# Kernel optimization log

Measured on AMD Instinct MI355X. Metric: run time of the kernel, lower is better.

Reference implementation:

```python
import jax, jax.numpy as jnp
import numpy as np

B, T, D, U, R = 64, 512, 256, 256, 4


def setup_inputs() -> dict:
    key = jax.random.key(0)
    ks = jax.random.split(key, 12)
    inputs = jax.random.normal(ks[0], (B, T, D), dtype=jnp.float32)
    # per-timestep dependency indices into past timesteps; must satisfy dep[t] <= t
    dependencies = jnp.minimum(
        jax.random.randint(ks[1], (T, R - 1), 0, T), jnp.arange(T)[:, None]
    ).astype(jnp.int32)
    mask = jax.random.randint(ks[2], (B, T), 0, 2).astype(jnp.int32)
    initial_states = jax.random.normal(ks[3], (R, B, U), dtype=jnp.float32) * 0.1
    s = 1.0 / np.sqrt(U)
    def w(k, shape):
        return jax.random.normal(k, shape, dtype=jnp.float32) * s
    return dict(
        inputs=inputs, dependencies=dependencies, mask=mask, initial_states=initial_states,
        Wz=w(ks[4], (D, U)), Wr=w(ks[5], (D, U)), Wh=w(ks[6], (D, U)),
        Uz=w(ks[7], (U, U)), Ur=w(ks[8], (U, U)), Uh=w(ks[9], (U, U)),
        bz=jnp.zeros((U,), jnp.float32), br=jnp.zeros((U,), jnp.float32), bh=jnp.zeros((U,), jnp.float32),
    )


def reference(inputs, dependencies, mask, initial_states, Wz, Wr, Wh, Uz, Ur, Uh, bz, br, bh):
    Bn, Tn, _ = inputs.shape
    Rn = initial_states.shape[0]
    Un = Uz.shape[0]

    x = jnp.swapaxes(inputs, 0, 1)              # [T, B, D]  (time_major swap)
    m = jnp.swapaxes(mask, 0, 1).astype(bool)   # [T, B]
    # dependencies[i] is consumed AFTER step i (sets states for step i+1) -> shift by one
    dep_in = jnp.concatenate(
        [jnp.zeros((1, dependencies.shape[1]), dependencies.dtype), dependencies[:-1]], axis=0
    )

    def cell(x_t, states):
        # states: [R, B, U]  (child-sum Graph-GRU over recurrent_size predecessor states)
        r = jax.nn.sigmoid(x_t @ Wr + states @ Ur + br)          # [R, B, U]
        h_sum = states.sum(0)                                    # [B, U]
        z = jax.nn.sigmoid(x_t @ Wz + h_sum @ Uz + bz)
        h_tilde = jnp.tanh(x_t @ Wh + (r * states).sum(0) @ Uh + bh)
        h = z * (h_sum / Rn) + (1.0 - z) * h_tilde
        return h  # GRU: output == new state

    def step(carry, xs):
        prev_out, prev_state, buf, t = carry
        x_t, m_t, dep_t = xs
        gathered = buf[dep_t]                                    # [R-1, B, U] irregular history gather
        cand = jnp.concatenate([prev_state[None], gathered], axis=0)
        states = jnp.where(t == 0, initial_states, cand)
        h = cell(x_t, states)
        mt = m_t[:, None]                                        # [B, 1]
        out_m = jnp.where(mt, h, prev_out)                       # masked output (pre_output carry)
        st_m = jnp.where(mt, h, prev_state)                      # masked state  (pre_states carry)
        buf = buf.at[t].set(st_m)                                # successive_states[t]
        return (out_m, st_m, buf, t + 1), out_m

    carry0 = (
        jnp.zeros((Bn, Un), inputs.dtype),
        jnp.zeros((Bn, Un), inputs.dtype),
        jnp.zeros((Tn, Bn, Un), inputs.dtype),
        jnp.array(0, jnp.int32),
    )
    (last_out, last_state, _, _), outs = jax.lax.scan(step, carry0, (x, m, dep_in))

    # zero_output_for_mask
    last_out = jnp.where(m[-1][:, None], last_out, jnp.zeros_like(last_out))
    outs = jnp.where(m[:, :, None], outs, jnp.zeros_like(outs))
    outputs = jnp.swapaxes(outs, 0, 1)                           # back to [B, T, U]
    return outputs, last_out, last_state
```

## Files before the change

kernel.cpp:

```cpp
#include <hip/hip_runtime.h>
#include <cstdint>
#include <cstddef>

#define BN 64
#define TN 512
#define DN 256
#define UN 256
#define NC 768
#define SLOTS (TN + 5)
#define ZSLOT (TN + 4)

#define WROWS_LDS 6
#define WROWS_REG 2
#define WROWS_STR 24

__device__ __forceinline__ float sigm(float x) {
  return 1.0f / (1.0f + __expf(-x));
}
__device__ __forceinline__ float tanh_fast(float x) {
  float e = __expf(-2.0f * x);
  return 2.0f / (1.0f + e) - 1.0f;
}

__global__ __launch_bounds__(256) void build_wcat(
    const float* __restrict__ Wr, const float* __restrict__ Wz, const float* __restrict__ Wh,
    const float* __restrict__ br, const float* __restrict__ bz, const float* __restrict__ bh,
    float* __restrict__ wcat, float* __restrict__ bias)
{
  int idx = blockIdx.x * 256 + threadIdx.x;
  if (idx < DN * NC) {
    int k = idx / NC, c = idx % NC;
    float v;
    if (c < 256)      v = Wr[k * UN + c];
    else if (c < 512) v = Wz[k * UN + (c - 256)];
    else              v = Wh[k * UN + (c - 512)];
    wcat[idx] = v;
  }
  if (idx < NC) {
    bias[idx] = (idx < 256) ? br[idx] : ((idx < 512) ? bz[idx - 256] : bh[idx - 512]);
  }
}

__global__ __launch_bounds__(256) void gemm_xw(
    const float* __restrict__ X, const float* __restrict__ Wc,
    const float* __restrict__ bias, float* __restrict__ P)
{
  __shared__ float As[32][68];
  __shared__ float Bs[32][64];
  const int tid = threadIdx.x;
  const int m0 = blockIdx.x * 64;
  const int n0 = blockIdx.y * 64;
  const int ty = tid >> 4, tx = tid & 15;
  float acc[4][4] = {};

  const int ar = tid >> 3;
  const int ak = (tid & 7) * 4;
  const int bk = tid >> 4;
  const int bn = (tid & 15) * 4;

  for (int k0 = 0; k0 < DN; k0 += 32) {
    float4 a0 = *(const float4*)(X + (size_t)(m0 + ar) * DN + k0 + ak);
    float4 a1 = *(const float4*)(X + (size_t)(m0 + 32 + ar) * DN + k0 + ak);
    As[ak + 0][ar] = a0.x; As[ak + 1][ar] = a0.y; As[ak + 2][ar] = a0.z; As[ak + 3][ar] = a0.w;
    As[ak + 0][32 + ar] = a1.x; As[ak + 1][32 + ar] = a1.y; As[ak + 2][32 + ar] = a1.z; As[ak + 3][32 + ar] = a1.w;
    *(float4*)&Bs[bk][bn]      = *(const float4*)(Wc + (size_t)(k0 + bk) * NC + n0 + bn);
    *(float4*)&Bs[bk + 16][bn] = *(const float4*)(Wc + (size_t)(k0 + bk + 16) * NC + n0 + bn);
    __syncthreads();
#pragma unroll
    for (int kk = 0; kk < 32; kk++) {
      float4 av = *(const float4*)&As[kk][ty * 4];
      float4 bv = *(const float4*)&Bs[kk][tx * 4];
      acc[0][0] += av.x * bv.x; acc[0][1] += av.x * bv.y; acc[0][2] += av.x * bv.z; acc[0][3] += av.x * bv.w;
      acc[1][0] += av.y * bv.x; acc[1][1] += av.y * bv.y; acc[1][2] += av.y * bv.z; acc[1][3] += av.y * bv.w;
      acc[2][0] += av.z * bv.x; acc[2][1] += av.z * bv.y; acc[2][2] += av.z * bv.z; acc[2][3] += av.z * bv.w;
      acc[3][0] += av.w * bv.x; acc[3][1] += av.w * bv.y; acc[3][2] += av.w * bv.z; acc[3][3] += av.w * bv.w;
    }
    __syncthreads();
  }
  float4 bb = *(const float4*)(bias + n0 + tx * 4);
#pragma unroll
  for (int i = 0; i < 4; i++) {
    float4 o;
    o.x = acc[i][0] + bb.x; o.y = acc[i][1] + bb.y;
    o.z = acc[i][2] + bb.z; o.w = acc[i][3] + bb.w;
    *(float4*)(P + (size_t)(m0 + ty * 4 + i) * NC + n0 + tx * 4) = o;
  }
}

__global__ __launch_bounds__(1024, 1) void recurrent_kernel(
    const float* __restrict__ P,
    const float* __restrict__ Ur, const float* __restrict__ Uz, const float* __restrict__ Uh,
    const int* __restrict__ dep, const int* __restrict__ mask,
    const float* __restrict__ init,
    float* __restrict__ out,
    float* __restrict__ buf_s, float* __restrict__ buf_pr, float* __restrict__ buf_pz)
{
  const int b = blockIdx.x;
  const int tid = threadIdx.x;
  const int g4 = tid >> 8;
  const int u  = tid & 255;
  const int wv = tid >> 6;
  const int mat = wv & 1;
  const int s   = wv >> 1;
  const int l   = tid & 63;

  float wh[64];
  {
    const float* pu = Uh + (size_t)(64 * g4) * UN + u;
#pragma unroll
    for (int kk = 0; kk < 64; kk++) wh[kk] = pu[(size_t)kk * UN];
  }
  const float* Um = mat ? Uz : Ur;
  float4 wrg0 = ((const float4*)Um)[(size_t)(32 * s + WROWS_LDS + 0) * 64 + l];
  float4 wrg1 = ((const float4*)Um)[(size_t)(32 * s + WROWS_LDS + 1) * 64 + l];

  __shared__ float4 wlds4[2][8][WROWS_LDS][64];
  __shared__ float ls[4][256], lpr[4][256], lpz[4][256];
  __shared__ float lxf[NC];
  __shared__ float rs[256], hs[256], zv[256];
  __shared__ float red0[4][256];
  __shared__ float redd[2][8][256];
  __shared__ float scur[256], prcur[256], pzcur[256];
  __shared__ int eff[TN], nxt[TN], mloc[TN];
  __shared__ int deploc[TN * 3];

  for (int i = tid; i < 2 * 8 * WROWS_LDS * 64; i += 1024) {
    int mm = i / (8 * WROWS_LDS * 64);
    int r2 = i % (8 * WROWS_LDS * 64);
    int ss = r2 / (WROWS_LDS * 64);
    int rr = (r2 / 64) % WROWS_LDS;
    int ll = i & 63;
    wlds4[mm][ss][rr][ll] = ((const float4*)(mm ? Uz : Ur))[(size_t)(32 * ss + rr) * 64 + ll];
  }
  for (int i = tid; i < TN; i += 1024) mloc[i] = mask[b * TN + i];
  for (int i = tid; i < TN * 3; i += 1024) deploc[i] = dep[i];

  const size_t bufBase = (size_t)b * SLOTS * UN;

  {
    float v = init[((size_t)g4 * BN + b) * UN + u];
    ls[g4][u] = v;
    buf_s[bufBase + (size_t)(TN + g4) * UN + u] = v;
    if (tid < 256) {
      scur[u] = 0.0f; prcur[u] = 0.0f; pzcur[u] = 0.0f;
      buf_s[bufBase + (size_t)ZSLOT * UN + u] = 0.0f;
      buf_pr[bufBase + (size_t)ZSLOT * UN + u] = 0.0f;
      buf_pz[bufBase + (size_t)ZSLOT * UN + u] = 0.0f;
    }
  }
  __syncthreads();

  if (tid == 0) {
    int e = ZSLOT;
    for (int t2 = 0; t2 < TN; t2++) { if (mloc[t2]) e = t2; eff[t2] = e; }
  } else if (tid == 64) {
    int e = TN;
    for (int t2 = TN - 1; t2 >= 0; t2--) { if (mloc[t2]) e = t2; nxt[t2] = e; }
  }

  auto projD = [&](const float* hsrc) {
    const float* hb = hsrc + 32 * s;
    float4 a = {0, 0, 0, 0};
#pragma unroll
    for (int r = 0; r < WROWS_LDS; r++) {
      float hk = hb[r];
      float4 w = wlds4[mat][s][r][l];
      a.x = fmaf(hk, w.x, a.x); a.y = fmaf(hk, w.y, a.y);
      a.z = fmaf(hk, w.z, a.z); a.w = fmaf(hk, w.w, a.w);
    }
    {
      float hk = hb[WROWS_LDS + 0];
      a.x = fmaf(hk, wrg0.x, a.x); a.y = fmaf(hk, wrg0.y, a.y);
      a.z = fmaf(hk, wrg0.z, a.z); a.w = fmaf(hk, wrg0.w, a.w);
    }
    {
      float hk = hb[WROWS_LDS + 1];
      a.x = fmaf(hk, wrg1.x, a.x); a.y = fmaf(hk, wrg1.y, a.y);
      a.z = fmaf(hk, wrg1.z, a.z); a.w = fmaf(hk, wrg1.w, a.w);
    }
    const float4* p = (const float4*)Um + (size_t)(32 * s + WROWS_LDS + WROWS_REG) * 64 + l;
#pragma unroll 8
    for (int kk = 0; kk < WROWS_STR; kk++) {
      float hk = hb[WROWS_LDS + WROWS_REG + kk];
      float4 w = p[(size_t)kk * 64];
      a.x = fmaf(hk, w.x, a.x); a.y = fmaf(hk, w.y, a.y);
      a.z = fmaf(hk, w.z, a.z); a.w = fmaf(hk, w.w, a.w);
    }
    *(float4*)&redd[mat][s][4 * l] = a;
  };

#pragma unroll 1
  for (int gg = 0; gg < 4; gg++) {
    projD(&ls[gg][0]);
    __syncthreads();
    if (tid < 512) {
      int mm = tid >> 8, c = tid & 255;
      float v = 0.0f;
#pragma unroll
      for (int q = 0; q < 8; q++) v += redd[mm][q][c];
      (mm ? buf_pz : buf_pr)[bufBase + (size_t)(TN + gg) * UN + c] = v;
    }
    __syncthreads();
  }

  const size_t outB = (size_t)b * TN * UN;
  const size_t pB = (size_t)b * TN * NC;
  bool havePre = false;
  float eLs = 0.0f, eLpr = 0.0f, eLpz = 0.0f, eLx = 0.0f;
  int eSrc = -2;

#pragma unroll 1
  for (int t = 0; t < TN; t++) {
    if (mloc[t] == 0) {
      if (tid < 256) out[outB + (size_t)t * UN + u] = 0.0f;
      continue;
    }
    if (!havePre) {
      if (t > 0 && g4 == 0) {
        ls[0][u] = scur[u]; lpr[0][u] = prcur[u]; lpz[0][u] = pzcur[u];
      } else {
        int src = (t == 0) ? (TN + g4) : eff[deploc[(t - 1) * 3 + (g4 - 1)]];
        size_t base = bufBase + (size_t)src * UN + u;
        ls[g4][u]  = buf_s[base];
        lpr[g4][u] = buf_pr[base];
        lpz[g4][u] = buf_pz[base];
      }
      if (tid < NC) lxf[tid] = P[pB + (size_t)t * NC + tid];
    }
    __syncthreads();
    if (tid < 256) {
      float s0 = ls[0][u], s1 = ls[1][u], s2 = ls[2][u], s3 = ls[3][u];
      float xr = lxf[u];
      rs[u] = sigm(xr + lpr[0][u]) * s0 + sigm(xr + lpr[1][u]) * s1
            + sigm(xr + lpr[2][u]) * s2 + sigm(xr + lpr[3][u]) * s3;
      hs[u] = (s0 + s1) + (s2 + s3);
      zv[u] = sigm(lxf[256 + u] + ((lpz[0][u] + lpz[1][u]) + (lpz[2][u] + lpz[3][u])));
    }
    __syncthreads();
    const int tn = (t + 1 < TN) ? nxt[t + 1] : TN;
    if (tn < TN) {
      if (g4 > 0) {
        eSrc = eff[deploc[(tn - 1) * 3 + (g4 - 1)]];
        if (eSrc != t) {
          size_t base = bufBase + (size_t)eSrc * UN + u;
          eLs = buf_s[base]; eLpr = buf_pr[base]; eLpz = buf_pz[base];
        }
      }
      if (tid < NC) eLx = P[pB + (size_t)tn * NC + tid];
    }
    {
      float a0 = 0, a1 = 0, a2 = 0, a3 = 0;
      const float4* v4 = (const float4*)&rs[64 * g4];
#pragma unroll
      for (int kk = 0; kk < 16; kk++) {
        float4 v = v4[kk];
        a0 += v.x * wh[4 * kk];     a1 += v.y * wh[4 * kk + 1];
        a2 += v.z * wh[4 * kk + 2]; a3 += v.w * wh[4 * kk + 3];
      }
      red0[g4][u] = (a0 + a1) + (a2 + a3);
    }
    __syncthreads();
    if (tid < 256) {
      float ht = tanh_fast(lxf[512 + u] + ((red0[0][u] + red0[1][u]) + (red0[2][u] + red0[3][u])));
      float z = zv[u];
      float h = z * hs[u] * 0.25f + (1.0f - z) * ht;
      scur[u] = h;
      out[outB + (size_t)t * UN + u] = h;
      buf_s[bufBase + (size_t)t * UN + u] = h;
    }
    __syncthreads();
    projD(scur);
    __syncthreads();
    if (tid < 256) {
      float prn = 0.0f, pzn = 0.0f;
#pragma unroll
      for (int q = 0; q < 8; q++) { prn += redd[0][q][u]; pzn += redd[1][q][u]; }
      prcur[u] = prn; pzcur[u] = pzn;
      buf_pr[bufBase + (size_t)t * UN + u] = prn;
      buf_pz[bufBase + (size_t)t * UN + u] = pzn;
      if (tn < TN) { ls[0][u] = scur[u]; lpr[0][u] = prn; lpz[0][u] = pzn; }
    } else if (tn < TN) {
      if (eSrc == t) {
        float prn = 0.0f, pzn = 0.0f;
#pragma unroll
        for (int q = 0; q < 8; q++) { prn += redd[0][q][u]; pzn += redd[1][q][u]; }
        ls[g4][u] = scur[u]; lpr[g4][u] = prn; lpz[g4][u] = pzn;
      } else {
        ls[g4][u] = eLs; lpr[g4][u] = eLpr; lpz[g4][u] = eLpz;
      }
    }
    if (tn < TN && tid < NC) lxf[tid] = eLx;
    havePre = (tn < TN);
  }

  if (tid < 256) {
    float lst = scur[u];
    out[(size_t)BN * TN * UN + (size_t)b * UN + u] = mloc[TN - 1] ? lst : 0.0f;
    out[(size_t)BN * TN * UN + (size_t)BN * UN + (size_t)b * UN + u] = lst;
  }
}

extern "C" void kernel_launch(void* const* d_in, const int* in_sizes, int n_in,
                              void* d_out, int out_size, void* d_ws, size_t ws_size,
                              hipStream_t stream) {
  const float* inputs       = (const float*)d_in[0];
  const int*   dependencies = (const int*)d_in[1];
  const int*   mask         = (const int*)d_in[2];
  const float* initial      = (const float*)d_in[3];
  const float* Wz = (const float*)d_in[4];
  const float* Wr = (const float*)d_in[5];
  const float* Wh = (const float*)d_in[6];
  const float* Uz = (const float*)d_in[7];
  const float* Ur = (const float*)d_in[8];
  const float* Uh = (const float*)d_in[9];
  const float* bz = (const float*)d_in[10];
  const float* br = (const float*)d_in[11];
  const float* bh = (const float*)d_in[12];

  float* out = (float*)d_out;
  float* ws  = (float*)d_ws;
  float* wcat    = ws;
  float* bias    = wcat + (size_t)DN * NC;
  float* precomp = bias + NC;
  float* buf_s   = precomp + (size_t)BN * TN * NC;
  float* buf_pr  = buf_s + (size_t)BN * SLOTS * UN;
  float* buf_pz  = buf_pr + (size_t)BN * SLOTS * UN;

  build_wcat<<<(DN * NC + 255) / 256, 256, 0, stream>>>(Wr, Wz, Wh, br, bz, bh, wcat, bias);
  gemm_xw<<<dim3(BN * TN / 64, NC / 64), 256, 0, stream>>>(inputs, wcat, bias, precomp);
  recurrent_kernel<<<BN, 1024, 0, stream>>>(precomp, Ur, Uz, Uh, dependencies, mask, initial,
                                            out, buf_s, buf_pr, buf_pz);
}
```

Before: 2.210 ms.

## Fuse h computation into projection via wave shuffles, drop state staging and barriers

Each wave now redundantly computes the new hidden values for its 32-row slice and broadcasts them with __shfl into the Ur/Uz projection. This removes one barrier and the scur round trip per step. The LDS staging of the four gathered states and the register prefetch of the next step's dependencies are removed. The first 256 threads now load dependency states directly from global memory at the start of each step, while the upper 512 threads prefetch the next step's input projection during the reduction. Launch bounds change to allow more waves per EU, and register-held weight rows are dropped. The trade-off is exposed global-load latency on the critical path for the gathered states, in exchange for fewer synchronisations.

```diff
diff --git a/kernel.cpp b/kernel.cpp
--- a/kernel.cpp
+++ b/kernel.cpp
@@ -9,10 +9,7 @@
 #define NC 768
 #define SLOTS (TN + 5)
 #define ZSLOT (TN + 4)
-
-#define WROWS_LDS 6
-#define WROWS_REG 2
-#define WROWS_STR 24
+#define WL 6
 
 __device__ __forceinline__ float sigm(float x) {
   return 1.0f / (1.0f + __expf(-x));
@@ -87,7 +84,7 @@
   }
 }
 
-__global__ __launch_bounds__(1024, 1) void recurrent_kernel(
+__global__ __launch_bounds__(1024, 4) void recurrent_kernel(
     const float* __restrict__ P,
     const float* __restrict__ Ur, const float* __restrict__ Uz, const float* __restrict__ Uh,
     const int* __restrict__ dep, const int* __restrict__ mask,
@@ -111,42 +108,34 @@
     for (int kk = 0; kk < 64; kk++) wh[kk] = pu[(size_t)kk * UN];
   }
   const float* Um = mat ? Uz : Ur;
-  float4 wrg0 = ((const float4*)Um)[(size_t)(32 * s + WROWS_LDS + 0) * 64 + l];
-  float4 wrg1 = ((const float4*)Um)[(size_t)(32 * s + WROWS_LDS + 1) * 64 + l];
-
-  __shared__ float4 wlds4[2][8][WROWS_LDS][64];
-  __shared__ float ls[4][256], lpr[4][256], lpz[4][256];
+
+  __shared__ float4 wlds[2][8][WL][64];
   __shared__ float lxf[NC];
   __shared__ float rs[256], hs[256], zv[256];
   __shared__ float red0[4][256];
   __shared__ float redd[2][8][256];
   __shared__ float scur[256], prcur[256], pzcur[256];
-  __shared__ int eff[TN], nxt[TN], mloc[TN];
+  __shared__ int eff[TN], nxt[TN + 1], mloc[TN];
   __shared__ int deploc[TN * 3];
 
-  for (int i = tid; i < 2 * 8 * WROWS_LDS * 64; i += 1024) {
-    int mm = i / (8 * WROWS_LDS * 64);
-    int r2 = i % (8 * WROWS_LDS * 64);
-    int ss = r2 / (WROWS_LDS * 64);
-    int rr = (r2 / 64) % WROWS_LDS;
+  for (int i = tid; i < 2 * 8 * WL * 64; i += 1024) {
+    int mm = i / (8 * WL * 64);
+    int r2 = i % (8 * WL * 64);
+    int ss = r2 / (WL * 64);
+    int rr = (r2 / 64) % WL;
     int ll = i & 63;
-    wlds4[mm][ss][rr][ll] = ((const float4*)(mm ? Uz : Ur))[(size_t)(32 * ss + rr) * 64 + ll];
+    wlds[mm][ss][rr][ll] = ((const float4*)(mm ? Uz : Ur))[(size_t)(32 * ss + rr) * 64 + ll];
   }
   for (int i = tid; i < TN; i += 1024) mloc[i] = mask[b * TN + i];
   for (int i = tid; i < TN * 3; i += 1024) deploc[i] = dep[i];
 
   const size_t bufBase = (size_t)b * SLOTS * UN;
 
-  {
-    float v = init[((size_t)g4 * BN + b) * UN + u];
-    ls[g4][u] = v;
-    buf_s[bufBase + (size_t)(TN + g4) * UN + u] = v;
-    if (tid < 256) {
-      scur[u] = 0.0f; prcur[u] = 0.0f; pzcur[u] = 0.0f;
-      buf_s[bufBase + (size_t)ZSLOT * UN + u] = 0.0f;
-      buf_pr[bufBase + (size_t)ZSLOT * UN + u] = 0.0f;
-      buf_pz[bufBase + (size_t)ZSLOT * UN + u] = 0.0f;
-    }
+  if (tid < 256) {
+    scur[u] = 0.0f; prcur[u] = 0.0f; pzcur[u] = 0.0f;
+    buf_s[bufBase + (size_t)ZSLOT * UN + u] = 0.0f;
+    buf_pr[bufBase + (size_t)ZSLOT * UN + u] = 0.0f;
+    buf_pz[bufBase + (size_t)ZSLOT * UN + u] = 0.0f;
   }
   __syncthreads();
 
@@ -154,44 +143,38 @@
     int e = ZSLOT;
     for (int t2 = 0; t2 < TN; t2++) { if (mloc[t2]) e = t2; eff[t2] = e; }
   } else if (tid == 64) {
+    nxt[TN] = TN;
     int e = TN;
     for (int t2 = TN - 1; t2 >= 0; t2--) { if (mloc[t2]) e = t2; nxt[t2] = e; }
   }
 
-  auto projD = [&](const float* hsrc) {
-    const float* hb = hsrc + 32 * s;
-    float4 a = {0, 0, 0, 0};
-#pragma unroll
-    for (int r = 0; r < WROWS_LDS; r++) {
-      float hk = hb[r];
-      float4 w = wlds4[mat][s][r][l];
-      a.x = fmaf(hk, w.x, a.x); a.y = fmaf(hk, w.y, a.y);
-      a.z = fmaf(hk, w.z, a.z); a.w = fmaf(hk, w.w, a.w);
-    }
-    {
-      float hk = hb[WROWS_LDS + 0];
-      a.x = fmaf(hk, wrg0.x, a.x); a.y = fmaf(hk, wrg0.y, a.y);
-      a.z = fmaf(hk, wrg0.z, a.z); a.w = fmaf(hk, wrg0.w, a.w);
-    }
-    {
-      float hk = hb[WROWS_LDS + 1];
-      a.x = fmaf(hk, wrg1.x, a.x); a.y = fmaf(hk, wrg1.y, a.y);
-      a.z = fmaf(hk, wrg1.z, a.z); a.w = fmaf(hk, wrg1.w, a.w);
-    }
-    const float4* p = (const float4*)Um + (size_t)(32 * s + WROWS_LDS + WROWS_REG) * 64 + l;
-#pragma unroll 8
-    for (int kk = 0; kk < WROWS_STR; kk++) {
-      float hk = hb[WROWS_LDS + WROWS_REG + kk];
-      float4 w = p[(size_t)kk * 64];
-      a.x = fmaf(hk, w.x, a.x); a.y = fmaf(hk, w.y, a.y);
-      a.z = fmaf(hk, w.z, a.z); a.w = fmaf(hk, w.w, a.w);
-    }
-    *(float4*)&redd[mat][s][4 * l] = a;
-  };
-
 #pragma unroll 1
   for (int gg = 0; gg < 4; gg++) {
-    projD(&ls[gg][0]);
+    if (tid < 256) {
+      float v = init[((size_t)gg * BN + b) * UN + u];
+      rs[u] = v;
+      buf_s[bufBase + (size_t)(TN + gg) * UN + u] = v;
+    }
+    __syncthreads();
+    {
+      float4 a = {0, 0, 0, 0};
+#pragma unroll
+      for (int r = 0; r < WL; r++) {
+        float hk = rs[32 * s + r];
+        float4 w = wlds[mat][s][r][l];
+        a.x = fmaf(hk, w.x, a.x); a.y = fmaf(hk, w.y, a.y);
+        a.z = fmaf(hk, w.z, a.z); a.w = fmaf(hk, w.w, a.w);
+      }
+      const float4* p = (const float4*)Um + (size_t)(32 * s + WL) * 64 + l;
+#pragma unroll
+      for (int r = 0; r < 32 - WL; r++) {
+        float hk = rs[32 * s + WL + r];
+        float4 w = p[(size_t)r * 64];
+        a.x = fmaf(hk, w.x, a.x); a.y = fmaf(hk, w.y, a.y);
+        a.z = fmaf(hk, w.z, a.z); a.w = fmaf(hk, w.w, a.w);
+      }
+      *(float4*)&redd[mat][s][4 * l] = a;
+    }
     __syncthreads();
     if (tid < 512) {
       int mm = tid >> 8, c = tid & 255;
@@ -205,9 +188,12 @@
 
   const size_t outB = (size_t)b * TN * UN;
   const size_t pB = (size_t)b * TN * NC;
-  bool havePre = false;
-  float eLs = 0.0f, eLpr = 0.0f, eLpz = 0.0f, eLx = 0.0f;
-  int eSrc = -2;
+
+  {
+    int t0 = nxt[0];
+    if (t0 < TN && tid < NC) lxf[tid] = P[pB + (size_t)t0 * NC + tid];
+  }
+  __syncthreads();
 
 #pragma unroll 1
   for (int t = 0; t < TN; t++) {
@@ -215,39 +201,27 @@
       if (tid < 256) out[outB + (size_t)t * UN + u] = 0.0f;
       continue;
     }
-    if (!havePre) {
-      if (t > 0 && g4 == 0) {
-        ls[0][u] = scur[u]; lpr[0][u] = prcur[u]; lpz[0][u] = pzcur[u];
+    if (tid < 256) {
+      float xr = lxf[u], xz = lxf[256 + u];
+      float s0, p0, q0;
+      if (t == 0) {
+        size_t base = bufBase + (size_t)(TN + 0) * UN + u;
+        s0 = buf_s[base]; p0 = buf_pr[base]; q0 = buf_pz[base];
       } else {
-        int src = (t == 0) ? (TN + g4) : eff[deploc[(t - 1) * 3 + (g4 - 1)]];
-        size_t base = bufBase + (size_t)src * UN + u;
-        ls[g4][u]  = buf_s[base];
-        lpr[g4][u] = buf_pr[base];
-        lpz[g4][u] = buf_pz[base];
-      }
-      if (tid < NC) lxf[tid] = P[pB + (size_t)t * NC + tid];
-    }
-    __syncthreads();
-    if (tid < 256) {
-      float s0 = ls[0][u], s1 = ls[1][u], s2 = ls[2][u], s3 = ls[3][u];
-      float xr = lxf[u];
-      rs[u] = sigm(xr + lpr[0][u]) * s0 + sigm(xr + lpr[1][u]) * s1
-            + sigm(xr + lpr[2][u]) * s2 + sigm(xr + lpr[3][u]) * s3;
+        s0 = scur[u]; p0 = prcur[u]; q0 = pzcur[u];
+      }
+      size_t b1 = bufBase + (size_t)((t == 0) ? (TN + 1) : eff[deploc[(t - 1) * 3 + 0]]) * UN + u;
+      size_t b2 = bufBase + (size_t)((t == 0) ? (TN + 2) : eff[deploc[(t - 1) * 3 + 1]]) * UN + u;
+      size_t b3 = bufBase + (size_t)((t == 0) ? (TN + 3) : eff[deploc[(t - 1) * 3 + 2]]) * UN + u;
+      float s1 = buf_s[b1], s2 = buf_s[b2], s3 = buf_s[b3];
+      float p1 = buf_pr[b1], p2 = buf_pr[b2], p3 = buf_pr[b3];
+      float q1 = buf_pz[b1], q2 = buf_pz[b2], q3 = buf_pz[b3];
+      rs[u] = sigm(xr + p0) * s0 + sigm(xr + p1) * s1
+            + sigm(xr + p2) * s2 + sigm(xr + p3) * s3;
       hs[u] = (s0 + s1) + (s2 + s3);
-      zv[u] = sigm(lxf[256 + u] + ((lpz[0][u] + lpz[1][u]) + (lpz[2][u] + lpz[3][u])));
-    }
-    __syncthreads();
-    const int tn = (t + 1 < TN) ? nxt[t + 1] : TN;
-    if (tn < TN) {
-      if (g4 > 0) {
-        eSrc = eff[deploc[(tn - 1) * 3 + (g4 - 1)]];
-        if (eSrc != t) {
-          size_t base = bufBase + (size_t)eSrc * UN + u;
-          eLs = buf_s[base]; eLpr = buf_pr[base]; eLpz = buf_pz[base];
-        }
-      }
-      if (tid < NC) eLx = P[pB + (size_t)tn * NC + tid];
-    }
+      zv[u] = sigm(xz + ((q0 + q1) + (q2 + q3)));
+    }
+    __syncthreads();
     {
       float a0 = 0, a1 = 0, a2 = 0, a3 = 0;
       const float4* v4 = (const float4*)&rs[64 * g4];
@@ -260,37 +234,51 @@
       red0[g4][u] = (a0 + a1) + (a2 + a3);
     }
     __syncthreads();
-    if (tid < 256) {
-      float ht = tanh_fast(lxf[512 + u] + ((red0[0][u] + red0[1][u]) + (red0[2][u] + red0[3][u])));
-      float z = zv[u];
-      float h = z * hs[u] * 0.25f + (1.0f - z) * ht;
-      scur[u] = h;
-      out[outB + (size_t)t * UN + u] = h;
-      buf_s[bufBase + (size_t)t * UN + u] = h;
-    }
-    __syncthreads();
-    projD(scur);
-    __syncthreads();
-    if (tid < 256) {
-      float prn = 0.0f, pzn = 0.0f;
-#pragma unroll
-      for (int q = 0; q < 8; q++) { prn += redd[0][q][u]; pzn += redd[1][q][u]; }
-      prcur[u] = prn; pzcur[u] = pzn;
-      buf_pr[bufBase + (size_t)t * UN + u] = prn;
-      buf_pz[bufBase + (size_t)t * UN + u] = pzn;
-      if (tn < TN) { ls[0][u] = scur[u]; lpr[0][u] = prn; lpz[0][u] = pzn; }
-    } else if (tn < TN) {
-      if (eSrc == t) {
-        float prn = 0.0f, pzn = 0.0f;
-#pragma unroll
-        for (int q = 0; q < 8; q++) { prn += redd[0][q][u]; pzn += redd[1][q][u]; }
-        ls[g4][u] = scur[u]; lpr[g4][u] = prn; lpz[g4][u] = pzn;
-      } else {
-        ls[g4][u] = eLs; lpr[g4][u] = eLpr; lpz[g4][u] = eLpz;
-      }
-    }
-    if (tn < TN && tid < NC) lxf[tid] = eLx;
-    havePre = (tn < TN);
+    {
+      int c = 32 * s + (l & 31);
+      float ht = tanh_fast(lxf[512 + c] + ((red0[0][c] + red0[1][c]) + (red0[2][c] + red0[3][c])));
+      float z = zv[c];
+      float hval = z * hs[c] * 0.25f + (1.0f - z) * ht;
+      if (mat == 0 && l < 32) {
+        scur[c] = hval;
+        out[outB + (size_t)t * UN + c] = hval;
+        buf_s[bufBase + (size_t)t * UN + c] = hval;
+      }
+      float4 a = {0, 0, 0, 0};
+#pragma unroll
+      for (int r = 0; r < WL; r++) {
+        float hk = __shfl(hval, r);
+        float4 w = wlds[mat][s][r][l];
+        a.x = fmaf(hk, w.x, a.x); a.y = fmaf(hk, w.y, a.y);
+        a.z = fmaf(hk, w.z, a.z); a.w = fmaf(hk, w.w, a.w);
+      }
+      const float4* p = (const float4*)Um + (size_t)(32 * s + WL) * 64 + l;
+#pragma unroll
+      for (int r = 0; r < 32 - WL; r++) {
+        float hk = __shfl(hval, WL + r);
+        float4 w = p[(size_t)r * 64];
+        a.x = fmaf(hk, w.x, a.x); a.y = fmaf(hk, w.y, a.y);
+        a.z = fmaf(hk, w.z, a.z); a.w = fmaf(hk, w.w, a.w);
+      }
+      *(float4*)&redd[mat][s][4 * l] = a;
+    }
+    __syncthreads();
+    if (tid < 512) {
+      int mm = tid >> 8, c = tid & 255;
+      float v = 0.0f;
+#pragma unroll
+      for (int q = 0; q < 8; q++) v += redd[mm][q][c];
+      if (mm == 0) { prcur[c] = v; buf_pr[bufBase + (size_t)t * UN + c] = v; }
+      else         { pzcur[c] = v; buf_pz[bufBase + (size_t)t * UN + c] = v; }
+    } else {
+      int tn = nxt[t + 1];
+      if (tn < TN) {
+        int i = tid - 512;
+        lxf[i] = P[pB + (size_t)tn * NC + i];
+        if (i < 256) lxf[512 + i] = P[pB + (size_t)tn * NC + 512 + i];
+      }
+    }
+    __syncthreads();
   }
 
   if (tid < 256) {
```

After: 4.670 ms. +111.3%, slower.
